# Optimization experiments

Measured on AMD Instinct MI355X. Metric: run time of the kernel, lower is better.

## Reference

```python
import jax, jax.numpy as jnp
import numpy as np


def setup_inputs() -> dict:
    key = jax.random.key(0)
    k1, k2, k3 = jax.random.split(key, 3)
    B, D, F = 4096, 1024, 16384  # batch, input_dim, dict_size
    x = jax.random.normal(k1, (B, D), dtype=jnp.float32)
    W_enc = jax.random.normal(k2, (F, D), dtype=jnp.float32) * (1.0 / np.sqrt(D))
    b_enc = jnp.zeros((F,), dtype=jnp.float32)
    W_dec = jax.random.normal(k3, (D, F), dtype=jnp.float32)
    # decoder columns are unit-normalized (as in _normalize_decoder)
    W_dec = W_dec / jnp.clip(jnp.linalg.norm(W_dec, axis=0, keepdims=True), 1e-8)
    b_dec = jnp.zeros((D,), dtype=jnp.float32)
    return {"x": x, "W_enc": W_enc, "b_enc": b_enc, "W_dec": W_dec, "b_dec": b_dec, "k": 32}


def reference(x, W_enc, b_enc, W_dec, b_dec, k):
    # encode: z_pre = (x - b_dec) @ W_enc^T + b_enc   -> [B, F]
    x_centered = x - b_dec
    z_pre = jnp.einsum('bd,fd->bf', x_centered, W_enc) + b_enc
    # activate: TopK(ReLU(z_pre)) via top_k + relu + scatter
    topk_vals, topk_idx = jax.lax.top_k(z_pre, k)           # [B, k]
    B = z_pre.shape[0]
    rows = jnp.arange(B)[:, None]                            # [B, 1]
    z = jnp.zeros_like(z_pre).at[rows, topk_idx].set(jax.nn.relu(topk_vals))
    # decode: x_hat = z @ W_dec^T + b_dec (dense matmul over sparse z)
    x_hat = jnp.einsum('bf,df->bd', z, W_dec) + b_dec
    return (x_hat, z, z_pre)
```

## Files before the change

kernel.cpp:

```cpp
#include <hip/hip_runtime.h>
#include <cstdint>
#include <cfloat>
#include <cstddef>

#define MAXK 128

typedef __attribute__((ext_vector_type(8))) short bf16x8;
typedef __attribute__((ext_vector_type(4))) float f32x4;

__device__ __forceinline__ void split8(const float4& v0, const float4& v1,
                                       uint4& hp, uint4& lp)
{
    float vv[8] = {v0.x, v0.y, v0.z, v0.w, v1.x, v1.y, v1.z, v1.w};
    unsigned h[8], l[8];
    #pragma unroll
    for (int i = 0; i < 8; ++i) {
        unsigned u  = __float_as_uint(vv[i]);
        unsigned hb = u & 0xFFFF0000u;
        float lf    = vv[i] - __uint_as_float(hb);
        h[i] = u;
        l[i] = __float_as_uint(lf);
    }
    hp.x = (h[0] >> 16) | (h[1] & 0xFFFF0000u);
    hp.y = (h[2] >> 16) | (h[3] & 0xFFFF0000u);
    hp.z = (h[4] >> 16) | (h[5] & 0xFFFF0000u);
    hp.w = (h[6] >> 16) | (h[7] & 0xFFFF0000u);
    lp.x = (l[0] >> 16) | (l[1] & 0xFFFF0000u);
    lp.y = (l[2] >> 16) | (l[3] & 0xFFFF0000u);
    lp.z = (l[4] >> 16) | (l[5] & 0xFFFF0000u);
    lp.w = (l[6] >> 16) | (l[7] & 0xFFFF0000u);
}

__device__ __forceinline__ void gload_lds16(const void* g, void* l)
{
    __builtin_amdgcn_global_load_lds(
        (const __attribute__((address_space(1))) unsigned int*)g,
        (__attribute__((address_space(3))) unsigned int*)l,
        16, 0, 0);
}

__global__ __launch_bounds__(256)
void prep_x_kernel(const float* __restrict__ x, const float* __restrict__ b_dec,
                   ushort* __restrict__ AhiP, ushort* __restrict__ AloP, int D)
{
    const int c   = blockIdx.x * 256 + threadIdx.x;
    const int t   = c >> 9;
    const int wc  = c & 511;
    const int rl  = wc >> 2;
    const int pkc = wc & 3;
    const int kc  = (pkc - (rl >> 1)) & 3;
    const int nkb = D >> 5;
    const int band = t / nkb, kblk = t - band * nkb;
    const int row = band * 128 + rl;
    const int k0  = kblk * 32 + kc * 8;

    const float* src = x + (size_t)row * D + k0;
    float4 v0 = *(const float4*)(src);
    float4 v1 = *(const float4*)(src + 4);
    const float* bd = b_dec + k0;
    float4 d0 = *(const float4*)(bd);
    float4 d1 = *(const float4*)(bd + 4);
    v0.x -= d0.x; v0.y -= d0.y; v0.z -= d0.z; v0.w -= d0.w;
    v1.x -= d1.x; v1.y -= d1.y; v1.z -= d1.z; v1.w -= d1.w;
    uint4 hp, lp;
    split8(v0, v1, hp, lp);
    const size_t off = (size_t)t * 4096 + (size_t)wc * 8;
    *(uint4*)&AhiP[off] = hp;
    *(uint4*)&AloP[off] = lp;
}

__global__ __launch_bounds__(256)
void prep_w_kernel(const float* __restrict__ Wenc,
                   ushort* __restrict__ WhiP, ushort* __restrict__ WloP, int D)
{
    const int c   = blockIdx.x * 256 + threadIdx.x;
    const int t   = c >> 10;
    const int wc  = c & 1023;
    const int rl  = wc >> 2;
    const int pkc = wc & 3;
    const int kc  = (pkc - (rl >> 1)) & 3;
    const int nkb = D >> 5;
    const int fband = t / nkb, kblk = t - fband * nkb;
    const int f   = fband * 256 + rl;
    const int k0  = kblk * 32 + kc * 8;

    const float* src = Wenc + (size_t)f * D + k0;
    float4 v0 = *(const float4*)(src);
    float4 v1 = *(const float4*)(src + 4);
    uint4 hp, lp;
    split8(v0, v1, hp, lp);
    const size_t off = (size_t)t * 8192 + (size_t)wc * 8;
    *(uint4*)&WhiP[off] = hp;
    *(uint4*)&WloP[off] = lp;
}

__global__ __launch_bounds__(256, 2)
void encode_gemm_pre(const ushort* __restrict__ AhiP, const ushort* __restrict__ AloP,
                     const ushort* __restrict__ WhiP, const ushort* __restrict__ WloP,
                     const float* __restrict__ b_enc, float* __restrict__ z_pre,
                     int D, int F)
{
    __shared__ ushort AsHi[4096];
    __shared__ ushort AsLo[4096];
    __shared__ ushort BsHi[8192];
    __shared__ ushort BsLo[8192];

    const int tid = threadIdx.x;
    const int bm  = blockIdx.y * 128;
    const int bn  = blockIdx.x * 256;

    const int lane = tid & 63;
    const int w    = tid >> 6;
    const int wm   = (w >> 1) * 64;
    const int wn   = (w & 1) * 128;
    const int fr   = lane & 15;
    const int q    = lane >> 4;
    const int nkb  = D >> 5;

    int aoff[4], boff[8];
    #pragma unroll
    for (int mi = 0; mi < 4; ++mi) {
        const int r = wm + mi * 16 + fr;
        aoff[mi] = r * 32 + (((q + (r >> 1)) & 3) * 8);
    }
    #pragma unroll
    for (int ni = 0; ni < 8; ++ni) {
        const int r = wn + ni * 16 + fr;
        boff[ni] = r * 32 + (((q + (r >> 1)) & 3) * 8);
    }

    f32x4 acc[4][8];
    #pragma unroll
    for (int mi = 0; mi < 4; ++mi)
        #pragma unroll
        for (int ni = 0; ni < 8; ++ni)
            acc[mi][ni] = (f32x4){0.f, 0.f, 0.f, 0.f};

    const char* aHi = (const char*)AhiP + (size_t)blockIdx.y * nkb * 8192;
    const char* aLo = (const char*)AloP + (size_t)blockIdx.y * nkb * 8192;
    const char* bHi = (const char*)WhiP + (size_t)blockIdx.x * nkb * 16384;
    const char* bLo = (const char*)WloP + (size_t)blockIdx.x * nkb * 16384;
    const int la16 = lane * 16;

    for (int kb = 0; kb < nkb; ++kb) {
        const char* pa = aHi + (size_t)kb * 8192;
        const char* pl = aLo + (size_t)kb * 8192;
        const char* pb = bHi + (size_t)kb * 16384;
        const char* pm = bLo + (size_t)kb * 16384;

        #pragma unroll
        for (int c = 0; c < 2; ++c) {
            const int off = (w * 2 + c) * 1024;
            gload_lds16(pa + off + la16, (char*)AsHi + off);
            gload_lds16(pl + off + la16, (char*)AsLo + off);
        }
        #pragma unroll
        for (int c = 0; c < 4; ++c) {
            const int off = (w * 4 + c) * 1024;
            gload_lds16(pb + off + la16, (char*)BsHi + off);
            gload_lds16(pm + off + la16, (char*)BsLo + off);
        }
        asm volatile("s_waitcnt vmcnt(0)" ::: "memory");
        __syncthreads();

        bf16x8 ahi[4], alo[4];
        #pragma unroll
        for (int mi = 0; mi < 4; ++mi) {
            ahi[mi] = *(const bf16x8*)&AsHi[aoff[mi]];
            alo[mi] = *(const bf16x8*)&AsLo[aoff[mi]];
        }
        #pragma unroll
        for (int ni = 0; ni < 8; ++ni) {
            bf16x8 bhi = *(const bf16x8*)&BsHi[boff[ni]];
            bf16x8 blo = *(const bf16x8*)&BsLo[boff[ni]];
            #pragma unroll
            for (int mi = 0; mi < 4; ++mi) {
                acc[mi][ni] = __builtin_amdgcn_mfma_f32_16x16x32_bf16(alo[mi], bhi, acc[mi][ni], 0, 0, 0);
                acc[mi][ni] = __builtin_amdgcn_mfma_f32_16x16x32_bf16(ahi[mi], blo, acc[mi][ni], 0, 0, 0);
                acc[mi][ni] = __builtin_amdgcn_mfma_f32_16x16x32_bf16(ahi[mi], bhi, acc[mi][ni], 0, 0, 0);
            }
        }
        __syncthreads();
    }

    #pragma unroll
    for (int ni = 0; ni < 8; ++ni) {
        const int col = bn + wn + ni * 16 + fr;
        const float be = b_enc[col];
        #pragma unroll
        for (int mi = 0; mi < 4; ++mi) {
            const int rbase = bm + wm + mi * 16 + q * 4;
            float* dst = z_pre + (size_t)rbase * F + col;
            #pragma unroll
            for (int r = 0; r < 4; ++r)
                dst[(size_t)r * F] = acc[mi][ni][r] + be;
        }
    }
}

__global__ __launch_bounds__(256, 2)
void encode_gemm_bf16x3(const float* __restrict__ x, const float* __restrict__ Wenc,
                        const float* __restrict__ b_enc, const float* __restrict__ b_dec,
                        float* __restrict__ z_pre, int D, int F)
{
    constexpr int BM = 128, BN = 256, BK = 32;
    __shared__ ushort AsHi[BM * BK];
    __shared__ ushort AsLo[BM * BK];
    __shared__ ushort BsHi[BN * BK];
    __shared__ ushort BsLo[BN * BK];

    const int tid = threadIdx.x;
    const int bm  = blockIdx.y * BM;
    const int bn  = blockIdx.x * BN;

    const int lane = tid & 63;
    const int w    = tid >> 6;
    const int wm   = (w >> 1) * 64;
    const int wn   = (w & 1) * 128;
    const int fr   = lane & 15;
    const int q    = lane >> 4;

    int aoff[4], boff[8];
    #pragma unroll
    for (int mi = 0; mi < 4; ++mi) {
        const int r = wm + mi * 16 + fr;
        aoff[mi] = r * 32 + (((q + (r >> 1)) & 3) * 8);
    }
    #pragma unroll
    for (int ni = 0; ni < 8; ++ni) {
        const int r = wn + ni * 16 + fr;
        boff[ni] = r * 32 + (((q + (r >> 1)) & 3) * 8);
    }

    f32x4 acc[4][8];
    #pragma unroll
    for (int mi = 0; mi < 4; ++mi)
        #pragma unroll
        for (int ni = 0; ni < 8; ++ni)
            acc[mi][ni] = (f32x4){0.f, 0.f, 0.f, 0.f};

    for (int k0 = 0; k0 < D; k0 += BK) {
        #pragma unroll
        for (int j = 0; j < 2; ++j) {
            const int task = tid + 256 * j;
            const int row = task >> 2, kc = task & 3;
            const float* src = x + (size_t)(bm + row) * D + k0 + kc * 8;
            float4 v0 = *(const float4*)(src);
            float4 v1 = *(const float4*)(src + 4);
            const float* bd = b_dec + k0 + kc * 8;
            float4 d0 = *(const float4*)(bd);
            float4 d1 = *(const float4*)(bd + 4);
            v0.x -= d0.x; v0.y -= d0.y; v0.z -= d0.z; v0.w -= d0.w;
            v1.x -= d1.x; v1.y -= d1.y; v1.z -= d1.z; v1.w -= d1.w;
            uint4 hp, lp;
            split8(v0, v1, hp, lp);
            const int off = row * 32 + (((kc + (row >> 1)) & 3) * 8);
            *(uint4*)&AsHi[off] = hp;
            *(uint4*)&AsLo[off] = lp;
        }
        #pragma unroll
        for (int j = 0; j < 4; ++j) {
            const int task = tid + 256 * j;
            const int row = task >> 2, kc = task & 3;
            const float* src = Wenc + (size_t)(bn + row) * D + k0 + kc * 8;
            float4 v0 = *(const float4*)(src);
            float4 v1 = *(const float4*)(src + 4);
            uint4 hp, lp;
            split8(v0, v1, hp, lp);
            const int off = row * 32 + (((kc + (row >> 1)) & 3) * 8);
            *(uint4*)&BsHi[off] = hp;
            *(uint4*)&BsLo[off] = lp;
        }
        __syncthreads();

        bf16x8 ahi[4], alo[4];
        #pragma unroll
        for (int mi = 0; mi < 4; ++mi) {
            ahi[mi] = *(const bf16x8*)&AsHi[aoff[mi]];
            alo[mi] = *(const bf16x8*)&AsLo[aoff[mi]];
        }
        #pragma unroll
        for (int ni = 0; ni < 8; ++ni) {
            bf16x8 bhi = *(const bf16x8*)&BsHi[boff[ni]];
            bf16x8 blo = *(const bf16x8*)&BsLo[boff[ni]];
            #pragma unroll
            for (int mi = 0; mi < 4; ++mi) {
                acc[mi][ni] = __builtin_amdgcn_mfma_f32_16x16x32_bf16(alo[mi], bhi, acc[mi][ni], 0, 0, 0);
                acc[mi][ni] = __builtin_amdgcn_mfma_f32_16x16x32_bf16(ahi[mi], blo, acc[mi][ni], 0, 0, 0);
                acc[mi][ni] = __builtin_amdgcn_mfma_f32_16x16x32_bf16(ahi[mi], bhi, acc[mi][ni], 0, 0, 0);
            }
        }
        __syncthreads();
    }

    #pragma unroll
    for (int ni = 0; ni < 8; ++ni) {
        const int col = bn + wn + ni * 16 + fr;
        const float be = b_enc[col];
        #pragma unroll
        for (int mi = 0; mi < 4; ++mi) {
            const int rbase = bm + wm + mi * 16 + q * 4;
            float* dst = z_pre + (size_t)rbase * F + col;
            #pragma unroll
            for (int r = 0; r < 4; ++r)
                dst[(size_t)r * F] = acc[mi][ni][r] + be;
        }
    }
}

__device__ __forceinline__ unsigned fkey(float f)
{
    unsigned u = __float_as_uint(f);
    return u ^ ((unsigned)((int)u >> 31) | 0x80000000u);
}
__device__ __forceinline__ float finv(unsigned k)
{
    unsigned u = (k & 0x80000000u) ? (k ^ 0x80000000u) : ~k;
    return __uint_as_float(u);
}

template <int NVEC>
__global__ __launch_bounds__(256)
void topk_kernel(const float* __restrict__ z_pre, float* __restrict__ z,
                 float* __restrict__ ws_vals, int* __restrict__ ws_idx,
                 const int* __restrict__ k_ptr,
                 const float* __restrict__ x, const float* __restrict__ Wenc,
                 const float* __restrict__ b_enc, const float* __restrict__ b_dec,
                 int F, int D)
{
    const int row = blockIdx.x;
    const int t   = threadIdx.x;
    const int k   = *k_ptr;
    const int nv4 = F >> 2;
    const int wv_id = t >> 6;
    const int ln    = t & 63;

    const float4* src = (const float4*)(z_pre + (size_t)row * F);
    float4 vals[NVEC];
    #pragma unroll
    for (int i = 0; i < NVEC; ++i) {
        const int p = t + 256 * i;
        if (p < nv4) vals[i] = src[p];
        else         vals[i] = make_float4(-FLT_MAX, -FLT_MAX, -FLT_MAX, -FLT_MAX);
    }

    __shared__ int hist[4][256];
    __shared__ int waveTot[4];
    __shared__ int s_bin, s_above;
    __shared__ int c_hi_s, n_c_s, out_cnt;
    __shared__ int cand_idx[128];
    __shared__ float cand_val[128];
    __shared__ unsigned char cand_sel[128];

    unsigned prefix = 0;
    int rem = k;

    #pragma unroll
    for (int pass = 0; pass < 2; ++pass) {
        const int shift = 24 - 8 * pass;
        hist[0][t] = 0; hist[1][t] = 0; hist[2][t] = 0; hist[3][t] = 0;
        __syncthreads();
        #pragma unroll
        for (int i = 0; i < NVEC; ++i) {
            const float* vv = (const float*)&vals[i];
            #pragma unroll
            for (int j = 0; j < 4; ++j) {
                const unsigned key = fkey(vv[j]);
                const bool inb = (pass == 0) || ((key >> (shift + 8)) == prefix);
                if (inb) atomicAdd(&hist[wv_id][(key >> shift) & 255], 1);
            }
        }
        __syncthreads();
        const int cnt = hist[0][t] + hist[1][t] + hist[2][t] + hist[3][t];
        int s = cnt;
        #pragma unroll
        for (int off = 1; off < 64; off <<= 1) {
            const int tmp = __shfl_down(s, off, 64);
            if (ln + off < 64) s += tmp;
        }
        if (ln == 0) waveTot[wv_id] = s;
        __syncthreads();
        int add = 0;
        #pragma unroll
        for (int w2 = 0; w2 < 4; ++w2)
            if (w2 > wv_id) add += waveTot[w2];
        const int sfx = s + add;
        const int nxt = sfx - cnt;
        if (sfx >= rem && nxt < rem) { s_bin = t; s_above = nxt; }
        __syncthreads();
        rem -= s_above;
        prefix = (prefix << 8) | (unsigned)s_bin;
        __syncthreads();
    }

    const unsigned keyLo = prefix << 16;
    const unsigned keyHi = keyLo | 0xFFFFu;
    const float dlt = 1e-3f;
    const float hiThr = finv(keyHi) + dlt;
    const float loThr = finv(keyLo) - dlt;

    if (t == 0) { c_hi_s = 0; n_c_s = 0; out_cnt = 0; }
    __syncthreads();

    #pragma unroll
    for (int i = 0; i < NVEC; ++i) {
        const float* vv = (const float*)&vals[i];
        #pragma unroll
        for (int j = 0; j < 4; ++j) {
            const float v = vv[j];
            if (v > hiThr) {
                atomicAdd(&c_hi_s, 1);
            } else if (v > loThr) {
                const int s = atomicAdd(&n_c_s, 1);
                if (s < 128) { cand_idx[s] = (t + 256 * i) * 4 + j; cand_sel[s] = 0; }
            }
        }
    }
    __syncthreads();

    const int n_c = min(n_c_s, 128);

    {
        const float* xr = x + (size_t)row * D;
        for (int c = wv_id; c < n_c; c += 4) {
            const int f = cand_idx[c];
            const float* wr = Wenc + (size_t)f * D;
            float s = 0.f;
            for (int d = ln * 4; d < D; d += 256) {
                float4 xv = *(const float4*)(xr + d);
                float4 bd = *(const float4*)(b_dec + d);
                float4 wv4 = *(const float4*)(wr + d);
                s = fmaf(xv.x - bd.x, wv4.x, s);
                s = fmaf(xv.y - bd.y, wv4.y, s);
                s = fmaf(xv.z - bd.z, wv4.z, s);
                s = fmaf(xv.w - bd.w, wv4.w, s);
            }
            #pragma unroll
            for (int o = 32; o > 0; o >>= 1) s += __shfl_down(s, o, 64);
            if (ln == 0) cand_val[c] = s + b_enc[f];
        }
    }
    __syncthreads();

    if (t == 0) {
        int need = k - c_hi_s;
        if (need > n_c) need = n_c;
        for (int it = 0; it < need; ++it) {
            int bi = -1; float bv = 0.f;
            for (int c = 0; c < n_c; ++c) {
                if (cand_sel[c]) continue;
                const float v = cand_val[c];
                if (bi < 0 || v > bv || (v == bv && cand_idx[c] < cand_idx[bi])) {
                    bi = c; bv = v;
                }
            }
            if (bi < 0) break;
            cand_sel[bi] = 1;
        }
    }
    __syncthreads();

    float4* dstz = (float4*)(z + (size_t)row * F);
    float*  wv   = ws_vals + (size_t)row * MAXK;
    int*    wi   = ws_idx  + (size_t)row * MAXK;

    #pragma unroll
    for (int i = 0; i < NVEC; ++i) {
        const int p4 = t + 256 * i;
        if (p4 < nv4) {
            const float* vv = (const float*)&vals[i];
            float4 outv;
            float* ov = (float*)&outv;
            #pragma unroll
            for (int j = 0; j < 4; ++j) {
                const int pos = p4 * 4 + j;
                const float v = vv[j];
                float zv = 0.f;
                bool sel = false;
                if (v > hiThr) {
                    zv = fmaxf(v, 0.f); sel = true;
                } else if (v > loThr) {
                    for (int c = 0; c < n_c; ++c) {
                        if (cand_idx[c] == pos) {
                            if (cand_sel[c]) { zv = fmaxf(cand_val[c], 0.f); sel = true; }
                            break;
                        }
                    }
                }
                ov[j] = zv;
                if (sel) {
                    const int s = atomicAdd(&out_cnt, 1);
                    if (s < MAXK) { wv[s] = zv; wi[s] = pos; }
                }
            }
            dstz[p4] = outv;
        }
    }
}

__global__ __launch_bounds__(256)
void transpose_kernel(const float* __restrict__ in, float* __restrict__ out,
                      int R, int C)
{
    __shared__ float tile[32][33];
    const int c0 = blockIdx.x * 32;
    const int r0 = blockIdx.y * 32;
    const int tx = threadIdx.x & 31;
    const int ty = threadIdx.x >> 5;

    #pragma unroll
    for (int i = ty; i < 32; i += 8) {
        const int r = r0 + i, c = c0 + tx;
        tile[i][tx] = (r < R && c < C) ? in[(size_t)r * C + c] : 0.f;
    }
    __syncthreads();
    #pragma unroll
    for (int i = ty; i < 32; i += 8) {
        const int c = c0 + i, r = r0 + tx;
        if (c < C && r < R) out[(size_t)c * R + r] = tile[tx][i];
    }
}

__global__ __launch_bounds__(256)
void decode_kernel(const float* __restrict__ WdT, const float* __restrict__ wvals,
                   const int* __restrict__ widx, const float* __restrict__ b_dec,
                   float* __restrict__ x_hat, const int* __restrict__ k_ptr, int D)
{
    __shared__ float sv[MAXK];
    __shared__ int   si[MAXK];
    const int row = blockIdx.x;
    const int t   = threadIdx.x;
    int k = *k_ptr;
    if (k > MAXK) k = MAXK;

    if (t < MAXK) {
        sv[t] = wvals[(size_t)row * MAXK + t];
        si[t] = widx [(size_t)row * MAXK + t];
    }
    __syncthreads();

    for (int d0 = t * 4; d0 < D; d0 += 1024) {
        float4 acc0 = *(const float4*)(b_dec + d0);
        float4 acc1 = make_float4(0.f, 0.f, 0.f, 0.f);
        int j = 0;
        for (; j + 2 <= k; j += 2) {
            const float v0 = sv[j],     v1 = sv[j + 1];
            const int   f0 = si[j],     f1 = si[j + 1];
            const float4 w0 = *(const float4*)(WdT + (size_t)f0 * D + d0);
            const float4 w1 = *(const float4*)(WdT + (size_t)f1 * D + d0);
            acc0.x = fmaf(v0, w0.x, acc0.x);
            acc0.y = fmaf(v0, w0.y, acc0.y);
            acc0.z = fmaf(v0, w0.z, acc0.z);
            acc0.w = fmaf(v0, w0.w, acc0.w);
            acc1.x = fmaf(v1, w1.x, acc1.x);
            acc1.y = fmaf(v1, w1.y, acc1.y);
            acc1.z = fmaf(v1, w1.z, acc1.z);
            acc1.w = fmaf(v1, w1.w, acc1.w);
        }
        if (j < k) {
            const float v0 = sv[j];
            const float4 w0 = *(const float4*)(WdT + (size_t)si[j] * D + d0);
            acc0.x = fmaf(v0, w0.x, acc0.x);
            acc0.y = fmaf(v0, w0.y, acc0.y);
            acc0.z = fmaf(v0, w0.z, acc0.z);
            acc0.w = fmaf(v0, w0.w, acc0.w);
        }
        acc0.x += acc1.x; acc0.y += acc1.y; acc0.z += acc1.z; acc0.w += acc1.w;
        *(float4*)(x_hat + (size_t)row * D + d0) = acc0;
    }
}

extern "C" void kernel_launch(void* const* d_in, const int* in_sizes, int n_in,
                              void* d_out, int out_size, void* d_ws, size_t ws_size,
                              hipStream_t stream)
{
    const float* x     = (const float*)d_in[0];
    const float* W_enc = (const float*)d_in[1];
    const float* b_enc = (const float*)d_in[2];
    const float* W_dec = (const float*)d_in[3];
    const float* b_dec = (const float*)d_in[4];
    const int*   k_ptr = (const int*)d_in[5];

    const int F = in_sizes[2];
    const int D = in_sizes[4];
    const int B = in_sizes[0] / D;

    float* x_hat = (float*)d_out;
    float* z     = x_hat + (size_t)B * D;
    float* z_pre = z + (size_t)B * F;

    float* WdT = (float*)d_ws;
    float* wv  = WdT + (size_t)F * D;
    int*   wi  = (int*)(wv + (size_t)B * MAXK);
    char*  extra = (char*)(wi + (size_t)B * MAXK);

    const size_t base_need  = (size_t)F * D * 4 + (size_t)B * MAXK * 8;
    const size_t extra_need = (size_t)B * D * 4 + (size_t)F * D * 4;
    const bool use_pre = (ws_size >= base_need + extra_need) &&
                         (D % 32 == 0) && (B % 128 == 0) && (F % 256 == 0);

    if (use_pre) {
        ushort* AhiP = (ushort*)extra;
        ushort* AloP = AhiP + (size_t)B * D;
        ushort* WhiP = AloP + (size_t)B * D;
        ushort* WloP = WhiP + (size_t)F * D;

        prep_x_kernel<<<(B * (D / 8)) / 256, 256, 0, stream>>>(x, b_dec, AhiP, AloP, D);
        prep_w_kernel<<<(F * (D / 8)) / 256, 256, 0, stream>>>(W_enc, WhiP, WloP, D);
        encode_gemm_pre<<<dim3(F / 256, B / 128), 256, 0, stream>>>(
            AhiP, AloP, WhiP, WloP, b_enc, z_pre, D, F);
    } else {
        encode_gemm_bf16x3<<<dim3(F / 256, B / 128), 256, 0, stream>>>(
            x, W_enc, b_enc, b_dec, z_pre, D, F);
    }

    transpose_kernel<<<dim3((F + 31) / 32, (D + 31) / 32), 256, 0, stream>>>(
        W_dec, WdT, D, F);

    const int nv4  = F / 4;
    const int nvec = (nv4 + 255) / 256;
    if (nvec <= 4)
        topk_kernel<4><<<B, 256, 0, stream>>>(z_pre, z, wv, wi, k_ptr, x, W_enc, b_enc, b_dec, F, D);
    else if (nvec <= 8)
        topk_kernel<8><<<B, 256, 0, stream>>>(z_pre, z, wv, wi, k_ptr, x, W_enc, b_enc, b_dec, F, D);
    else if (nvec <= 16)
        topk_kernel<16><<<B, 256, 0, stream>>>(z_pre, z, wv, wi, k_ptr, x, W_enc, b_enc, b_dec, F, D);
    else
        topk_kernel<32><<<B, 256, 0, stream>>>(z_pre, z, wv, wi, k_ptr, x, W_enc, b_enc, b_dec, F, D);

    decode_kernel<<<B, 256, 0, stream>>>(WdT, wv, wi, b_dec, x_hat, k_ptr, D);
}
```

Before: 1.229 ms.

## Add statistical-threshold top-k kernel with radix-select fallback

Adds a new top-k kernel that stores 16-bit keys of each z_pre row in shared memory. It estimates a selection threshold from the row's RMS via a Gaussian quantile approximation, gathers candidates above it, and ranks them with an O(n^2) count in shared memory. Only values within a small band around the k-th value are recomputed in exact fp32. When the estimate fails, it falls back to a two-pass radix select over the row. This is meant to replace the multi-pass scans of the old kernel, at the cost of heavy shared-memory use (32KB of keys), which can lower occupancy, and a reliance on roughly Gaussian activations to stay on the fast path.

```diff
diff --git a/kernel.cpp b/kernel.cpp
--- a/kernel.cpp
+++ b/kernel.cpp
@@ -319,6 +319,301 @@
     return __uint_as_float(u);
 }
 
+__device__ __forceinline__ float exact_zpre(const float* __restrict__ xr,
+                                            const float* __restrict__ Wenc,
+                                            const float* __restrict__ b_enc,
+                                            const float* __restrict__ b_dec,
+                                            int f, int D, int ln)
+{
+    const float* wr = Wenc + (size_t)f * D;
+    float s = 0.f;
+    for (int d = ln * 4; d < D; d += 256) {
+        float4 xv = *(const float4*)(xr + d);
+        float4 bd = *(const float4*)(b_dec + d);
+        float4 wv4 = *(const float4*)(wr + d);
+        s = fmaf(xv.x - bd.x, wv4.x, s);
+        s = fmaf(xv.y - bd.y, wv4.y, s);
+        s = fmaf(xv.z - bd.z, wv4.z, s);
+        s = fmaf(xv.w - bd.w, wv4.w, s);
+    }
+    #pragma unroll
+    for (int o = 32; o > 0; o >>= 1) s += __shfl_down(s, o, 64);
+    return s + b_enc[f];
+}
+
+#define DLT 4e-3f
+
+template <int NVEC>
+__global__ __launch_bounds__(256)
+void topk_fast(const float* __restrict__ z_pre, float* __restrict__ z,
+               float* __restrict__ ws_vals, int* __restrict__ ws_idx,
+               const int* __restrict__ k_ptr,
+               const float* __restrict__ x, const float* __restrict__ Wenc,
+               const float* __restrict__ b_enc, const float* __restrict__ b_dec,
+               int F, int D)
+{
+    const int row = blockIdx.x;
+    const int t   = threadIdx.x;
+    const int k   = *k_ptr;
+    const int nv4 = F >> 2;
+    const int wv_id = t >> 6, ln = t & 63;
+
+    __shared__ ushort keys[16384];
+    __shared__ float  cand_v[256];
+    __shared__ int    cand_i[256];
+    __shared__ unsigned char cand_sel[256];
+    __shared__ int    bnd[128];
+    __shared__ float  s2w[4];
+    __shared__ int    hist4[4][256];
+    __shared__ int    waveTot[4];
+    __shared__ int    s_bin, s_above;
+    __shared__ int    n_c_s, n_b_s, c_hi_s, out_cnt, cnt_tau_s, bad_s;
+    __shared__ unsigned vk_key;
+
+    if (t == 0) {
+        n_c_s = 0; n_b_s = 0; c_hi_s = 0; out_cnt = 0; cnt_tau_s = 0; bad_s = 0;
+        vk_key = 0xFFFFFFFFu;
+    }
+
+    const float*  zrow = z_pre + (size_t)row * F;
+    const float4* src  = (const float4*)zrow;
+
+    float s2 = 0.f;
+    #pragma unroll
+    for (int i = 0; i < NVEC; ++i) {
+        const int p = t + 256 * i;
+        if (p < nv4) {
+            const float4 v = src[p];
+            const unsigned k0 = fkey(v.x) >> 16;
+            const unsigned k1 = fkey(v.y) >> 16;
+            const unsigned k2 = fkey(v.z) >> 16;
+            const unsigned k3 = fkey(v.w) >> 16;
+            uint2 pk;
+            pk.x = k0 | (k1 << 16);
+            pk.y = k2 | (k3 << 16);
+            *(uint2*)&keys[p * 4] = pk;
+            s2 = fmaf(v.x, v.x, s2);
+            s2 = fmaf(v.y, v.y, s2);
+            s2 = fmaf(v.z, v.z, s2);
+            s2 = fmaf(v.w, v.w, s2);
+        }
+    }
+    #pragma unroll
+    for (int o = 32; o > 0; o >>= 1) s2 += __shfl_down(s2, o, 64);
+    if (ln == 0) s2w[wv_id] = s2;
+    __syncthreads();
+
+    const float sigma = sqrtf((s2w[0] + s2w[1] + s2w[2] + s2w[3]) / (float)F);
+    int c0 = 4 * k; if (c0 < 64) c0 = 64; if (c0 > 192) c0 = 192;
+    const float qq  = (float)c0 / (float)F;
+    const float tt  = sqrtf(-2.f * logf(qq));
+    const float phi = tt - (2.30753f + 0.27061f * tt) /
+                           (1.f + 0.99229f * tt + 0.04481f * tt * tt);
+    const float tau = sigma * phi;
+    const unsigned tk = fkey(tau) >> 16;
+    const unsigned tkey16 = (tk >= 2) ? (tk - 2) : 0;
+
+    const int nU = nv4 * 2;
+    const unsigned* keysU = (const unsigned*)keys;
+    for (int j = t; j < nU; j += 256) {
+        const unsigned pr = keysU[j];
+        const unsigned ka = pr & 0xFFFFu, kb = pr >> 16;
+        if (ka > tkey16) { const int s = atomicAdd(&n_c_s, 1); if (s < 256) cand_i[s] = 2 * j; }
+        if (kb > tkey16) { const int s = atomicAdd(&n_c_s, 1); if (s < 256) cand_i[s] = 2 * j + 1; }
+    }
+    __syncthreads();
+
+    if (t == 0 && (n_c_s > 256 || !(tau > 0.1f))) bad_s = 1;
+    const int n_c = min(n_c_s, 256);
+
+    float myv = 0.f;
+    if (t < n_c) {
+        myv = zrow[cand_i[t]];
+        cand_v[t] = myv;
+        if (myv > tau) atomicAdd(&cnt_tau_s, 1);
+    }
+    __syncthreads();
+    if (t == 0 && cnt_tau_s < k) bad_s = 1;
+
+    cand_sel[t] = 0;
+    if (t < n_c) {
+        int gt = 0;
+        for (int j = 0; j < n_c; ++j) gt += (cand_v[j] > myv);
+        if (gt <= k - 1) atomicMin(&vk_key, fkey(myv));
+    }
+    __syncthreads();
+
+    const float vkv = finv(vk_key);
+    if (t < n_c) {
+        if (myv > vkv + DLT) {
+            cand_sel[t] = 2;
+            atomicAdd(&c_hi_s, 1);
+        } else if (myv > vkv - DLT) {
+            const int sb = atomicAdd(&n_b_s, 1);
+            if (sb < 128) bnd[sb] = t;
+        }
+    }
+    __syncthreads();
+    if (t == 0 && n_b_s > 128) bad_s = 1;
+    __syncthreads();
+
+    if (!bad_s) {
+        const int n_b = n_b_s;
+        const float* xr = x + (size_t)row * D;
+        for (int b2 = wv_id; b2 < n_b; b2 += 4) {
+            const int c = bnd[b2];
+            const float ex = exact_zpre(xr, Wenc, b_enc, b_dec, cand_i[c], D, ln);
+            if (ln == 0) cand_v[c] = ex;
+        }
+        __syncthreads();
+
+        if (t == 0) {
+            int need = k - c_hi_s;
+            if (need > n_b) need = n_b;
+            for (int it = 0; it < need; ++it) {
+                int bi = -1; float bv = 0.f;
+                for (int b2 = 0; b2 < n_b; ++b2) {
+                    const int c = bnd[b2];
+                    if (cand_sel[c]) continue;
+                    const float v = cand_v[c];
+                    if (bi < 0 || v > bv || (v == bv && cand_i[c] < cand_i[bi])) {
+                        bi = c; bv = v;
+                    }
+                }
+                if (bi < 0) break;
+                cand_sel[bi] = 1;
+            }
+        }
+        __syncthreads();
+
+        float4* dstz = (float4*)(z + (size_t)row * F);
+        const float4 zz = make_float4(0.f, 0.f, 0.f, 0.f);
+        #pragma unroll
+        for (int i = 0; i < NVEC; ++i) {
+            const int p = t + 256 * i;
+            if (p < nv4) dstz[p] = zz;
+        }
+        __syncthreads();
+
+        float* wvp = ws_vals + (size_t)row * MAXK;
+        int*   wip = ws_idx  + (size_t)row * MAXK;
+        if (t < n_c && cand_sel[t]) {
+            const float zv = fmaxf(cand_v[t], 0.f);
+            z[(size_t)row * F + cand_i[t]] = zv;
+            const int s = atomicAdd(&out_cnt, 1);
+            if (s < MAXK) { wvp[s] = zv; wip[s] = cand_i[t]; }
+        }
+        return;
+    }
+
+    if (t == 0) { n_c_s = 0; c_hi_s = 0; out_cnt = 0; }
+    __syncthreads();
+
+    unsigned prefix = 0;
+    int rem = k;
+    for (int pass = 0; pass < 2; ++pass) {
+        const int shift = 24 - 8 * pass;
+        hist4[0][t] = 0; hist4[1][t] = 0; hist4[2][t] = 0; hist4[3][t] = 0;
+        __syncthreads();
+        for (int j = t; j < F; j += 256) {
+            const unsigned key = fkey(zrow[j]);
+            const bool inb = (pass == 0) || ((key >> (shift + 8)) == prefix);
+            if (inb) atomicAdd(&hist4[wv_id][(key >> shift) & 255], 1);
+        }
+        __syncthreads();
+        const int cnt = hist4[0][t] + hist4[1][t] + hist4[2][t] + hist4[3][t];
+        int s = cnt;
+        #pragma unroll
+        for (int off = 1; off < 64; off <<= 1) {
+            const int tmp = __shfl_down(s, off, 64);
+            if (ln + off < 64) s += tmp;
+        }
+        if (ln == 0) waveTot[wv_id] = s;
+        __syncthreads();
+        int add = 0;
+        #pragma unroll
+        for (int w2 = 0; w2 < 4; ++w2)
+            if (w2 > wv_id) add += waveTot[w2];
+        const int sfx = s + add;
+        const int nxt = sfx - cnt;
+        if (sfx >= rem && nxt < rem) { s_bin = t; s_above = nxt; }
+        __syncthreads();
+        rem -= s_above;
+        prefix = (prefix << 8) | (unsigned)s_bin;
+        __syncthreads();
+    }
+
+    const float hiT = finv((prefix << 16) | 0xFFFFu) + DLT;
+    const float loT = finv(prefix << 16) - DLT;
+
+    for (int j = t; j < F; j += 256) {
+        const float v = zrow[j];
+        if (v > hiT) atomicAdd(&c_hi_s, 1);
+        else if (v > loT) {
+            const int s = atomicAdd(&n_c_s, 1);
+            if (s < 256) { cand_i[s] = j; cand_sel[s] = 0; }
+        }
+    }
+    __syncthreads();
+    const int n_c2 = min(n_c_s, 256);
+
+    {
+        const float* xr = x + (size_t)row * D;
+        for (int c = wv_id; c < n_c2; c += 4) {
+            const float ex = exact_zpre(xr, Wenc, b_enc, b_dec, cand_i[c], D, ln);
+            if (ln == 0) cand_v[c] = ex;
+        }
+    }
+    __syncthreads();
+
+    if (t == 0) {
+        int need = k - c_hi_s;
+        if (need > n_c2) need = n_c2;
+        for (int it = 0; it < need; ++it) {
+            int bi = -1; float bv = 0.f;
+            for (int c = 0; c < n_c2; ++c) {
+                if (cand_sel[c]) continue;
+                const float v = cand_v[c];
+                if (bi < 0 || v > bv || (v == bv && cand_i[c] < cand_i[bi])) {
+                    bi = c; bv = v;
+                }
+            }
+            if (bi < 0) break;
+            cand_sel[bi] = 1;
+        }
+    }
+    __syncthreads();
+
+    {
+        float4* dstz = (float4*)(z + (size_t)row * F);
+        const float4 zz = make_float4(0.f, 0.f, 0.f, 0.f);
+        #pragma unroll
+        for (int i = 0; i < NVEC; ++i) {
+            const int p = t + 256 * i;
+            if (p < nv4) dstz[p] = zz;
+        }
+    }
+    __syncthreads();
+
+    float* wvp = ws_vals + (size_t)row * MAXK;
+    int*   wip = ws_idx  + (size_t)row * MAXK;
+    for (int j = t; j < F; j += 256) {
+        const float v = zrow[j];
+        if (v > hiT) {
+            const float zv = fmaxf(v, 0.f);
+            z[(size_t)row * F + j] = zv;
+            const int s = atomicAdd(&out_cnt, 1);
+            if (s < MAXK) { wvp[s] = zv; wip[s] = j; }
+        }
+    }
+    if (t < n_c2 && cand_sel[t]) {
+        const float zv = fmaxf(cand_v[t], 0.f);
+        z[(size_t)row * F + cand_i[t]] = zv;
+        const int s = atomicAdd(&out_cnt, 1);
+        if (s < MAXK) { wvp[s] = zv; wip[s] = cand_i[t]; }
+    }
+}
+
 template <int NVEC>
 __global__ __launch_bounds__(256)
 void topk_kernel(const float* __restrict__ z_pre, float* __restrict__ z,
@@ -423,21 +718,8 @@
     {
         const float* xr = x + (size_t)row * D;
         for (int c = wv_id; c < n_c; c += 4) {
-            const int f = cand_idx[c];
-            const float* wr = Wenc + (size_t)f * D;
-            float s = 0.f;
-            for (int d = ln * 4; d < D; d += 256) {
-                float4 xv = *(const float4*)(xr + d);
-                float4 bd = *(const float4*)(b_dec + d);
-                float4 wv4 = *(const float4*)(wr + d);
-                s = fmaf(xv.x - bd.x, wv4.x, s);
-                s = fmaf(xv.y - bd.y, wv4.y, s);
-                s = fmaf(xv.z - bd.z, wv4.z, s);
-                s = fmaf(xv.w - bd.w, wv4.w, s);
-            }
-            #pragma unroll
-            for (int o = 32; o > 0; o >>= 1) s += __shfl_down(s, o, 64);
-            if (ln == 0) cand_val[c] = s + b_enc[f];
+            const float ex = exact_zpre(xr, Wenc, b_enc, b_dec, cand_idx[c], D, ln);
+            if (ln == 0) cand_val[c] = ex;
         }
     }
     __syncthreads();
@@ -619,14 +901,23 @@
 
     const int nv4  = F / 4;
     const int nvec = (nv4 + 255) / 256;
-    if (nvec <= 4)
-        topk_kernel<4><<<B, 256, 0, stream>>>(z_pre, z, wv, wi, k_ptr, x, W_enc, b_enc, b_dec, F, D);
-    else if (nvec <= 8)
-        topk_kernel<8><<<B, 256, 0, stream>>>(z_pre, z, wv, wi, k_ptr, x, W_enc, b_enc, b_dec, F, D);
-    else if (nvec <= 16)
-        topk_kernel<16><<<B, 256, 0, stream>>>(z_pre, z, wv, wi, k_ptr, x, W_enc, b_enc, b_dec, F, D);
-    else
-        topk_kernel<32><<<B, 256, 0, stream>>>(z_pre, z, wv, wi, k_ptr, x, W_enc, b_enc, b_dec, F, D);
+    const bool fastok = (F <= 16384) && ((F & 3) == 0);
+
+    if (fastok) {
+        if (nvec <= 4)
+            topk_fast<4><<<B, 256, 0, stream>>>(z_pre, z, wv, wi, k_ptr, x, W_enc, b_enc, b_dec, F, D);
+        else if (nvec <= 8)
+            topk_fast<8><<<B, 256, 0, stream>>>(z_pre, z, wv, wi, k_ptr, x, W_enc, b_enc, b_dec, F, D);
+        else
+            topk_fast<16><<<B, 256, 0, stream>>>(z_pre, z, wv, wi, k_ptr, x, W_enc, b_enc, b_dec, F, D);
+    } else {
+        if (nvec <= 8)
+            topk_kernel<8><<<B, 256, 0, stream>>>(z_pre, z, wv, wi, k_ptr, x, W_enc, b_enc, b_dec, F, D);
+        else if (nvec <= 16)
+            topk_kernel<16><<<B, 256, 0, stream>>>(z_pre, z, wv, wi, k_ptr, x, W_enc, b_enc, b_dec, F, D);
+        else
+            topk_kernel<32><<<B, 256, 0, stream>>>(z_pre, z, wv, wi, k_ptr, x, W_enc, b_enc, b_dec, F, D);
+    }
 
     decode_kernel<<<B, 256, 0, stream>>>(WdT, wv, wi, b_dec, x_hat, k_ptr, D);
 }
```

After: 1.119 ms. 9.0% less time.
